# Kernel tuning notes

Hardware: AMD Instinct MI355X
Metric: run time of the kernel (lower is better)

Reference implementation:

```python
import jax, jax.numpy as jnp
import numpy as np

N_NODES, FEAT, EMB, BATCH, NUM_SAMPLE = 100000, 256, 256, 10000, 32


def setup_inputs() -> dict:
    key = jax.random.key(0)
    ks = jax.random.split(key, 8)
    sc = 1.0 / np.sqrt(FEAT).astype(np.float32)
    return {
        "nodes": jax.random.randint(ks[0], (BATCH,), 0, N_NODES),
        "neigh_idx": jax.random.randint(ks[1], (BATCH, NUM_SAMPLE), 0, N_NODES),
        "id2feat": jax.random.normal(ks[2], (N_NODES, FEAT), jnp.float32),
        "Wq": jax.random.normal(ks[3], (FEAT, EMB), jnp.float32) * sc,
        "bq": jnp.zeros((EMB,), jnp.float32),
        "Wk": jax.random.normal(ks[4], (FEAT, EMB), jnp.float32) * sc,
        "bk": jnp.zeros((EMB,), jnp.float32),
        "Wv": jax.random.normal(ks[5], (FEAT, EMB), jnp.float32) * sc,
        "bv": jnp.zeros((EMB,), jnp.float32),
    }


def reference(nodes, neigh_idx, id2feat, Wq, bq, Wk, bk, Wv, bv):
    # Gather: self feats [B, F] and sampled neighbor feats [B, S, F]
    self_feats = id2feat[nodes]
    neigh_feats = id2feat[neigh_idx]
    S = neigh_idx.shape[1]
    # Keys/values over [neighbors, self] -> [B, S+1, F]
    cat = jnp.concatenate([neigh_feats, self_feats[:, None, :]], axis=1)
    Q = self_feats @ Wq + bq               # [B, E]
    K = cat @ Wk + bk                       # [B, S+1, E]
    V = cat @ Wv + bv                       # [B, S+1, E]
    scores = jnp.einsum('be,bse->bs', Q, K)  # [B, S+1]
    # Faithful to original mask loop: with full neighbor lists, columns >= num_sample
    # (the appended self key) are masked out.
    mask = jnp.arange(S + 1) >= S
    scores = jnp.where(mask[None, :], -jnp.inf, scores)
    attn = jax.nn.softmax(scores, axis=-1)   # [B, S+1]
    return jnp.einsum('bs,bse->be', attn, V)  # [B, E]
```

## Files before the change

### kernel.cpp

```cpp
#include <hip/hip_runtime.h>
#include <math.h>

#define F 256
#define E 256
#define S 32
#define CH 4
#define LDK 40

typedef __attribute__((ext_vector_type(8))) short short8;
typedef __attribute__((ext_vector_type(4))) float f32x4;

__device__ __forceinline__ ushort f2bf(float x) {
    uint u = __float_as_uint(x);
    uint r = (u + 0x7fffu + ((u >> 16) & 1u)) >> 16;
    return (ushort)r;
}
__device__ __forceinline__ float bf2f(ushort h) {
    return __uint_as_float(((uint)h) << 16);
}

__global__ __launch_bounds__(256) void prep_all(const float* __restrict__ Wq,
                                                const float* __restrict__ bq,
                                                const float* __restrict__ Wk,
                                                const float* __restrict__ Wv,
                                                ushort* __restrict__ MT_hi,
                                                ushort* __restrict__ MT_lo,
                                                ushort* __restrict__ WvT_hi,
                                                ushort* __restrict__ WvT_lo,
                                                float* __restrict__ c) {
    const int t = threadIdx.x;
    if (blockIdx.x < 256) {
        const int j = blockIdx.x;
        __shared__ float wkj[F];
        wkj[t] = Wk[j * F + t];
        __syncthreads();
        float acc = 0.f;
#pragma unroll 8
        for (int e = 0; e < F; e += 4) {
            float4 wq = *reinterpret_cast<const float4*>(&Wq[t * E + e]);
            acc += wkj[e] * wq.x + wkj[e + 1] * wq.y + wkj[e + 2] * wq.z + wkj[e + 3] * wq.w;
        }
        const ushort hi = f2bf(acc);
        MT_hi[j * F + t] = hi;
        MT_lo[j * F + t] = f2bf(acc - bf2f(hi));
        if (t == 0) {
            float s = 0.f;
            for (int e = 0; e < F; ++e) s += wkj[e] * bq[e];
            c[j] = s;
        }
    } else {
        const int j = blockIdx.x - 256;
        const float v = Wv[t * E + j];
        const ushort hi = f2bf(v);
        WvT_hi[j * F + t] = hi;
        WvT_lo[j * F + t] = f2bf(v - bf2f(hi));
    }
}

__global__ __launch_bounds__(256) void mfma_gemm(const float* __restrict__ X,
                                                 const int* __restrict__ idx,
                                                 const ushort* __restrict__ BTh,
                                                 const ushort* __restrict__ BTl,
                                                 const float* __restrict__ bias,
                                                 float* __restrict__ out,
                                                 int rows) {
    __shared__ ushort Ah[64][LDK], Al[64][LDK];
    __shared__ ushort Bh[256][LDK], Bl[256][LDK];

    const int tid = threadIdx.x;
    const int lane = tid & 63, wave = tid >> 6;
    const int wm = wave >> 1, wn = wave & 1;
    const int fr = lane & 15, fk = lane >> 4;
    const int row0 = blockIdx.x * 64;

    const int arL = tid >> 2;
    const int akL = (tid & 3) * 8;
    const int ar = row0 + arL;
    const int arc = ar < rows ? ar : rows - 1;
    const long arow = idx ? (long)idx[arc] : (long)arc;
    const float* aptr = X + arow * (long)F + akL;

    const ushort* bhp = BTh + (size_t)tid * F;
    const ushort* blp = BTl + (size_t)tid * F;

    f32x4 acc[2][8];
#pragma unroll
    for (int m = 0; m < 2; ++m)
#pragma unroll
        for (int n = 0; n < 8; ++n) acc[m][n] = (f32x4){0.f, 0.f, 0.f, 0.f};

    for (int k0 = 0; k0 < F; k0 += 32) {
        const float4 v0 = *reinterpret_cast<const float4*>(&aptr[k0]);
        const float4 v1 = *reinterpret_cast<const float4*>(&aptr[k0 + 4]);
        const uint4 bh0 = *reinterpret_cast<const uint4*>(&bhp[k0]);
        const uint4 bh1 = *reinterpret_cast<const uint4*>(&bhp[k0 + 8]);
        const uint4 bh2 = *reinterpret_cast<const uint4*>(&bhp[k0 + 16]);
        const uint4 bh3 = *reinterpret_cast<const uint4*>(&bhp[k0 + 24]);
        const uint4 bl0 = *reinterpret_cast<const uint4*>(&blp[k0]);
        const uint4 bl1 = *reinterpret_cast<const uint4*>(&blp[k0 + 8]);
        const uint4 bl2 = *reinterpret_cast<const uint4*>(&blp[k0 + 16]);
        const uint4 bl3 = *reinterpret_cast<const uint4*>(&blp[k0 + 24]);

        const float xv[8] = {v0.x, v0.y, v0.z, v0.w, v1.x, v1.y, v1.z, v1.w};
        ushort h[8], l[8];
#pragma unroll
        for (int jj = 0; jj < 8; ++jj) {
            h[jj] = f2bf(xv[jj]);
            l[jj] = f2bf(xv[jj] - bf2f(h[jj]));
        }
        uint4 ph, pl;
        ph.x = (uint)h[0] | ((uint)h[1] << 16); ph.y = (uint)h[2] | ((uint)h[3] << 16);
        ph.z = (uint)h[4] | ((uint)h[5] << 16); ph.w = (uint)h[6] | ((uint)h[7] << 16);
        pl.x = (uint)l[0] | ((uint)l[1] << 16); pl.y = (uint)l[2] | ((uint)l[3] << 16);
        pl.z = (uint)l[4] | ((uint)l[5] << 16); pl.w = (uint)l[6] | ((uint)l[7] << 16);

        __syncthreads();
        *reinterpret_cast<uint4*>(&Ah[arL][akL]) = ph;
        *reinterpret_cast<uint4*>(&Al[arL][akL]) = pl;
        *reinterpret_cast<uint4*>(&Bh[tid][0])  = bh0;
        *reinterpret_cast<uint4*>(&Bh[tid][8])  = bh1;
        *reinterpret_cast<uint4*>(&Bh[tid][16]) = bh2;
        *reinterpret_cast<uint4*>(&Bh[tid][24]) = bh3;
        *reinterpret_cast<uint4*>(&Bl[tid][0])  = bl0;
        *reinterpret_cast<uint4*>(&Bl[tid][8])  = bl1;
        *reinterpret_cast<uint4*>(&Bl[tid][16]) = bl2;
        *reinterpret_cast<uint4*>(&Bl[tid][24]) = bl3;
        __syncthreads();

        const short8 a_h0 = *reinterpret_cast<const short8*>(&Ah[wm * 32 + fr][fk * 8]);
        const short8 a_l0 = *reinterpret_cast<const short8*>(&Al[wm * 32 + fr][fk * 8]);
        const short8 a_h1 = *reinterpret_cast<const short8*>(&Ah[wm * 32 + 16 + fr][fk * 8]);
        const short8 a_l1 = *reinterpret_cast<const short8*>(&Al[wm * 32 + 16 + fr][fk * 8]);
#pragma unroll
        for (int n = 0; n < 8; ++n) {
            const short8 b_h = *reinterpret_cast<const short8*>(&Bh[wn * 128 + n * 16 + fr][fk * 8]);
            const short8 b_l = *reinterpret_cast<const short8*>(&Bl[wn * 128 + n * 16 + fr][fk * 8]);
            acc[0][n] = __builtin_amdgcn_mfma_f32_16x16x32_bf16(a_h0, b_h, acc[0][n], 0, 0, 0);
            acc[0][n] = __builtin_amdgcn_mfma_f32_16x16x32_bf16(a_h0, b_l, acc[0][n], 0, 0, 0);
            acc[0][n] = __builtin_amdgcn_mfma_f32_16x16x32_bf16(a_l0, b_h, acc[0][n], 0, 0, 0);
            acc[1][n] = __builtin_amdgcn_mfma_f32_16x16x32_bf16(a_h1, b_h, acc[1][n], 0, 0, 0);
            acc[1][n] = __builtin_amdgcn_mfma_f32_16x16x32_bf16(a_h1, b_l, acc[1][n], 0, 0, 0);
            acc[1][n] = __builtin_amdgcn_mfma_f32_16x16x32_bf16(a_l1, b_h, acc[1][n], 0, 0, 0);
        }
    }

#pragma unroll
    for (int n = 0; n < 8; ++n) {
        const int col = wn * 128 + n * 16 + fr;
        const float bb = bias[col];
#pragma unroll
        for (int m = 0; m < 2; ++m) {
#pragma unroll
            for (int r = 0; r < 4; ++r) {
                const int orow = row0 + wm * 32 + m * 16 + fk * 4 + r;
                if (orow < rows)
                    out[(size_t)orow * E + col] = acc[m][n][r] + bb;
            }
        }
    }
}

__device__ __forceinline__ void ld_chunk(float4* d, int idxv, int s0,
                                         const float* __restrict__ t, int lane) {
#pragma unroll
    for (int j = 0; j < CH; ++j) {
        const int nid = __builtin_amdgcn_readlane(idxv, s0 + j);
        d[j] = *reinterpret_cast<const float4*>(&t[(size_t)nid * F + lane * 4]);
    }
}

__device__ __forceinline__ void proc_chunk(const float4* v, const float4 qv,
                                           float& m, float& l, float4& acc) {
#pragma unroll
    for (int j = 0; j < CH; ++j) {
        float p = v[j].x * qv.x + v[j].y * qv.y + v[j].z * qv.z + v[j].w * qv.w;
#pragma unroll
        for (int off = 32; off; off >>= 1) p += __shfl_xor(p, off);
        if (p <= m) {
            const float w = __expf(p - m);
            l += w;
            acc.x += w * v[j].x; acc.y += w * v[j].y;
            acc.z += w * v[j].z; acc.w += w * v[j].w;
        } else {
            const float c = __expf(m - p);
            l = l * c + 1.f;
            acc.x = acc.x * c + v[j].x; acc.y = acc.y * c + v[j].y;
            acc.z = acc.z * c + v[j].z; acc.w = acc.w * c + v[j].w;
            m = p;
        }
    }
}

__global__ __launch_bounds__(256) void attn_gather(const int* __restrict__ neigh_idx,
                                                   const float* __restrict__ id2feat,
                                                   float* __restrict__ qtm,
                                                   int B) {
    const int node = blockIdx.x * 4 + (threadIdx.x >> 6);
    const int lane = threadIdx.x & 63;
    if (node >= B) return;

    const int idxv = neigh_idx[node * S + (lane & (S - 1))];
    const float4 qv = *reinterpret_cast<const float4*>(&qtm[(size_t)node * F + lane * 4]);

    float m = -INFINITY, l = 0.f;
    float4 acc = make_float4(0.f, 0.f, 0.f, 0.f);

    float4 va[CH], vb[CH];
    ld_chunk(va, idxv, 0, id2feat, lane);
    ld_chunk(vb, idxv, 4, id2feat, lane);
    proc_chunk(va, qv, m, l, acc);
    ld_chunk(va, idxv, 8, id2feat, lane);
    proc_chunk(vb, qv, m, l, acc);
    ld_chunk(vb, idxv, 12, id2feat, lane);
    proc_chunk(va, qv, m, l, acc);
    ld_chunk(va, idxv, 16, id2feat, lane);
    proc_chunk(vb, qv, m, l, acc);
    ld_chunk(vb, idxv, 20, id2feat, lane);
    proc_chunk(va, qv, m, l, acc);
    ld_chunk(va, idxv, 24, id2feat, lane);
    proc_chunk(vb, qv, m, l, acc);
    ld_chunk(vb, idxv, 28, id2feat, lane);
    proc_chunk(va, qv, m, l, acc);
    proc_chunk(vb, qv, m, l, acc);

    const float inv = 1.0f / l;
    float4 o;
    o.x = acc.x * inv; o.y = acc.y * inv; o.z = acc.z * inv; o.w = acc.w * inv;
    *reinterpret_cast<float4*>(&qtm[(size_t)node * F + lane * 4]) = o;
}

extern "C" void kernel_launch(void* const* d_in, const int* in_sizes, int n_in,
                              void* d_out, int out_size, void* d_ws, size_t ws_size,
                              hipStream_t stream) {
    const int*   nodes   = (const int*)d_in[0];
    const int*   neigh   = (const int*)d_in[1];
    const float* id2feat = (const float*)d_in[2];
    const float* Wq      = (const float*)d_in[3];
    const float* bq      = (const float*)d_in[4];
    const float* Wk      = (const float*)d_in[5];
    const float* Wv      = (const float*)d_in[7];
    const float* bv      = (const float*)d_in[8];
    float* out = (float*)d_out;
    const int B = in_sizes[0];

    ushort* MT_hi  = (ushort*)d_ws;
    ushort* MT_lo  = MT_hi + 65536;
    ushort* WvT_hi = MT_lo + 65536;
    ushort* WvT_lo = WvT_hi + 65536;
    float*  cbuf   = (float*)(WvT_lo + 65536);
    float*  qtm    = cbuf + 256;

    prep_all<<<dim3(512), dim3(256), 0, stream>>>(Wq, bq, Wk, Wv,
                                                  MT_hi, MT_lo, WvT_hi, WvT_lo, cbuf);
    mfma_gemm<<<dim3((B + 63) / 64), dim3(256), 0, stream>>>(id2feat, nodes,
                                                             MT_hi, MT_lo, cbuf, qtm, B);
    attn_gather<<<dim3((B + 3) / 4), dim3(256), 0, stream>>>(neigh, id2feat, qtm, B);
    mfma_gemm<<<dim3((B + 63) / 64), dim3(256), 0, stream>>>(qtm, nullptr,
                                                             WvT_hi, WvT_lo, bv, out, B);
}
```

Before: 122.5 us.

## Compute Wk·Wqᵀ via MFMA GEMM, split prep kernel, widen GEMM blocks to 512 threads

```diff
diff --git a/kernel.cpp b/kernel.cpp
--- a/kernel.cpp
+++ b/kernel.cpp
@@ -12,151 +12,190 @@
 
 __device__ __forceinline__ ushort f2bf(float x) {
     uint u = __float_as_uint(x);
-    uint r = (u + 0x7fffu + ((u >> 16) & 1u)) >> 16;
-    return (ushort)r;
+    return (ushort)((u + 0x7fffu + ((u >> 16) & 1u)) >> 16);
 }
 __device__ __forceinline__ float bf2f(ushort h) {
     return __uint_as_float(((uint)h) << 16);
 }
-
-__global__ __launch_bounds__(256) void prep_all(const float* __restrict__ Wq,
-                                                const float* __restrict__ bq,
-                                                const float* __restrict__ Wk,
-                                                const float* __restrict__ Wv,
-                                                ushort* __restrict__ MT_hi,
-                                                ushort* __restrict__ MT_lo,
-                                                ushort* __restrict__ WvT_hi,
-                                                ushort* __restrict__ WvT_lo,
-                                                float* __restrict__ c) {
-    const int t = threadIdx.x;
-    if (blockIdx.x < 256) {
-        const int j = blockIdx.x;
-        __shared__ float wkj[F];
-        wkj[t] = Wk[j * F + t];
-        __syncthreads();
-        float acc = 0.f;
-#pragma unroll 8
-        for (int e = 0; e < F; e += 4) {
-            float4 wq = *reinterpret_cast<const float4*>(&Wq[t * E + e]);
-            acc += wkj[e] * wq.x + wkj[e + 1] * wq.y + wkj[e + 2] * wq.z + wkj[e + 3] * wq.w;
-        }
-        const ushort hi = f2bf(acc);
-        MT_hi[j * F + t] = hi;
-        MT_lo[j * F + t] = f2bf(acc - bf2f(hi));
-        if (t == 0) {
-            float s = 0.f;
-            for (int e = 0; e < F; ++e) s += wkj[e] * bq[e];
-            c[j] = s;
-        }
-    } else {
-        const int j = blockIdx.x - 256;
-        const float v = Wv[t * E + j];
-        const ushort hi = f2bf(v);
-        WvT_hi[j * F + t] = hi;
-        WvT_lo[j * F + t] = f2bf(v - bf2f(hi));
-    }
-}
-
-__global__ __launch_bounds__(256) void mfma_gemm(const float* __restrict__ X,
+__device__ __forceinline__ void split4(const float* x, uint2& ph, uint2& pl) {
+    ushort h[4], l[4];
+#pragma unroll
+    for (int i = 0; i < 4; ++i) { h[i] = f2bf(x[i]); l[i] = f2bf(x[i] - bf2f(h[i])); }
+    ph.x = (uint)h[0] | ((uint)h[1] << 16); ph.y = (uint)h[2] | ((uint)h[3] << 16);
+    pl.x = (uint)l[0] | ((uint)l[1] << 16); pl.y = (uint)l[2] | ((uint)l[3] << 16);
+}
+__device__ __forceinline__ uint4 pack8(const ushort* h) {
+    uint4 r;
+    r.x = (uint)h[0] | ((uint)h[1] << 16); r.y = (uint)h[2] | ((uint)h[3] << 16);
+    r.z = (uint)h[4] | ((uint)h[5] << 16); r.w = (uint)h[6] | ((uint)h[7] << 16);
+    return r;
+}
+
+template<bool INSPLIT, bool OUTSPLIT>
+__global__ __launch_bounds__(512) void mfma_gemm(const float* __restrict__ X,
                                                  const int* __restrict__ idx,
                                                  const ushort* __restrict__ BTh,
                                                  const ushort* __restrict__ BTl,
+                                                 const float* __restrict__ Bf,
                                                  const float* __restrict__ bias,
                                                  float* __restrict__ out,
+                                                 ushort* __restrict__ outh,
+                                                 ushort* __restrict__ outl,
                                                  int rows) {
     __shared__ ushort Ah[64][LDK], Al[64][LDK];
     __shared__ ushort Bh[256][LDK], Bl[256][LDK];
 
     const int tid = threadIdx.x;
     const int lane = tid & 63, wave = tid >> 6;
-    const int wm = wave >> 1, wn = wave & 1;
+    const int wm = wave >> 2, wn = wave & 3;
     const int fr = lane & 15, fk = lane >> 4;
     const int row0 = blockIdx.x * 64;
 
-    const int arL = tid >> 2;
-    const int akL = (tid & 3) * 8;
+    const int arL = tid >> 3;
+    const int akL = (tid & 7) * 4;
     const int ar = row0 + arL;
     const int arc = ar < rows ? ar : rows - 1;
     const long arow = idx ? (long)idx[arc] : (long)arc;
     const float* aptr = X + arow * (long)F + akL;
 
-    const ushort* bhp = BTh + (size_t)tid * F;
-    const ushort* blp = BTl + (size_t)tid * F;
-
-    f32x4 acc[2][8];
+    const int bcol = tid & 255;
+    const int bkh = (tid >> 8) * 16;
+
+    f32x4 acc[2][4];
 #pragma unroll
     for (int m = 0; m < 2; ++m)
 #pragma unroll
-        for (int n = 0; n < 8; ++n) acc[m][n] = (f32x4){0.f, 0.f, 0.f, 0.f};
+        for (int n = 0; n < 4; ++n) acc[m][n] = (f32x4){0.f, 0.f, 0.f, 0.f};
 
     for (int k0 = 0; k0 < F; k0 += 32) {
-        const float4 v0 = *reinterpret_cast<const float4*>(&aptr[k0]);
-        const float4 v1 = *reinterpret_cast<const float4*>(&aptr[k0 + 4]);
-        const uint4 bh0 = *reinterpret_cast<const uint4*>(&bhp[k0]);
-        const uint4 bh1 = *reinterpret_cast<const uint4*>(&bhp[k0 + 8]);
-        const uint4 bh2 = *reinterpret_cast<const uint4*>(&bhp[k0 + 16]);
-        const uint4 bh3 = *reinterpret_cast<const uint4*>(&bhp[k0 + 24]);
-        const uint4 bl0 = *reinterpret_cast<const uint4*>(&blp[k0]);
-        const uint4 bl1 = *reinterpret_cast<const uint4*>(&blp[k0 + 8]);
-        const uint4 bl2 = *reinterpret_cast<const uint4*>(&blp[k0 + 16]);
-        const uint4 bl3 = *reinterpret_cast<const uint4*>(&blp[k0 + 24]);
-
-        const float xv[8] = {v0.x, v0.y, v0.z, v0.w, v1.x, v1.y, v1.z, v1.w};
-        ushort h[8], l[8];
-#pragma unroll
-        for (int jj = 0; jj < 8; ++jj) {
-            h[jj] = f2bf(xv[jj]);
-            l[jj] = f2bf(xv[jj] - bf2f(h[jj]));
-        }
-        uint4 ph, pl;
-        ph.x = (uint)h[0] | ((uint)h[1] << 16); ph.y = (uint)h[2] | ((uint)h[3] << 16);
-        ph.z = (uint)h[4] | ((uint)h[5] << 16); ph.w = (uint)h[6] | ((uint)h[7] << 16);
-        pl.x = (uint)l[0] | ((uint)l[1] << 16); pl.y = (uint)l[2] | ((uint)l[3] << 16);
-        pl.z = (uint)l[4] | ((uint)l[5] << 16); pl.w = (uint)l[6] | ((uint)l[7] << 16);
+        const float4 av = *reinterpret_cast<const float4*>(&aptr[k0]);
+        uint2 ah, al;
+        split4(&av.x, ah, al);
+
+        uint4 wh0, wh1, wl0, wl1;
+        if constexpr (INSPLIT) {
+            const float* bp = Bf + (size_t)bcol * F + k0 + bkh;
+            float4 b0 = *reinterpret_cast<const float4*>(bp);
+            float4 b1 = *reinterpret_cast<const float4*>(bp + 4);
+            float4 b2 = *reinterpret_cast<const float4*>(bp + 8);
+            float4 b3 = *reinterpret_cast<const float4*>(bp + 12);
+            uint2 h0, l0, h1, l1, h2, l2, h3, l3;
+            split4(&b0.x, h0, l0); split4(&b1.x, h1, l1);
+            split4(&b2.x, h2, l2); split4(&b3.x, h3, l3);
+            wh0 = make_uint4(h0.x, h0.y, h1.x, h1.y);
+            wh1 = make_uint4(h2.x, h2.y, h3.x, h3.y);
+            wl0 = make_uint4(l0.x, l0.y, l1.x, l1.y);
+            wl1 = make_uint4(l2.x, l2.y, l3.x, l3.y);
+        } else {
+            const ushort* bph = BTh + (size_t)bcol * F + k0 + bkh;
+            const ushort* bpl = BTl + (size_t)bcol * F + k0 + bkh;
+            wh0 = *reinterpret_cast<const uint4*>(bph);
+            wh1 = *reinterpret_cast<const uint4*>(bph + 8);
+            wl0 = *reinterpret_cast<const uint4*>(bpl);
+            wl1 = *reinterpret_cast<const uint4*>(bpl + 8);
+        }
 
         __syncthreads();
-        *reinterpret_cast<uint4*>(&Ah[arL][akL]) = ph;
-        *reinterpret_cast<uint4*>(&Al[arL][akL]) = pl;
-        *reinterpret_cast<uint4*>(&Bh[tid][0])  = bh0;
-        *reinterpret_cast<uint4*>(&Bh[tid][8])  = bh1;
-        *reinterpret_cast<uint4*>(&Bh[tid][16]) = bh2;
-        *reinterpret_cast<uint4*>(&Bh[tid][24]) = bh3;
-        *reinterpret_cast<uint4*>(&Bl[tid][0])  = bl0;
-        *reinterpret_cast<uint4*>(&Bl[tid][8])  = bl1;
-        *reinterpret_cast<uint4*>(&Bl[tid][16]) = bl2;
-        *reinterpret_cast<uint4*>(&Bl[tid][24]) = bl3;
+        *reinterpret_cast<uint2*>(&Ah[arL][akL]) = ah;
+        *reinterpret_cast<uint2*>(&Al[arL][akL]) = al;
+        *reinterpret_cast<uint4*>(&Bh[bcol][bkh]) = wh0;
+        *reinterpret_cast<uint4*>(&Bh[bcol][bkh + 8]) = wh1;
+        *reinterpret_cast<uint4*>(&Bl[bcol][bkh]) = wl0;
+        *reinterpret_cast<uint4*>(&Bl[bcol][bkh + 8]) = wl1;
         __syncthreads();
 
-        const short8 a_h0 = *reinterpret_cast<const short8*>(&Ah[wm * 32 + fr][fk * 8]);
-        const short8 a_l0 = *reinterpret_cast<const short8*>(&Al[wm * 32 + fr][fk * 8]);
-        const short8 a_h1 = *reinterpret_cast<const short8*>(&Ah[wm * 32 + 16 + fr][fk * 8]);
-        const short8 a_l1 = *reinterpret_cast<const short8*>(&Al[wm * 32 + 16 + fr][fk * 8]);
-#pragma unroll
-        for (int n = 0; n < 8; ++n) {
-            const short8 b_h = *reinterpret_cast<const short8*>(&Bh[wn * 128 + n * 16 + fr][fk * 8]);
-            const short8 b_l = *reinterpret_cast<const short8*>(&Bl[wn * 128 + n * 16 + fr][fk * 8]);
-            acc[0][n] = __builtin_amdgcn_mfma_f32_16x16x32_bf16(a_h0, b_h, acc[0][n], 0, 0, 0);
-            acc[0][n] = __builtin_amdgcn_mfma_f32_16x16x32_bf16(a_h0, b_l, acc[0][n], 0, 0, 0);
-            acc[0][n] = __builtin_amdgcn_mfma_f32_16x16x32_bf16(a_l0, b_h, acc[0][n], 0, 0, 0);
-            acc[1][n] = __builtin_amdgcn_mfma_f32_16x16x32_bf16(a_h1, b_h, acc[1][n], 0, 0, 0);
-            acc[1][n] = __builtin_amdgcn_mfma_f32_16x16x32_bf16(a_h1, b_l, acc[1][n], 0, 0, 0);
-            acc[1][n] = __builtin_amdgcn_mfma_f32_16x16x32_bf16(a_l1, b_h, acc[1][n], 0, 0, 0);
-        }
-    }
-
-#pragma unroll
-    for (int n = 0; n < 8; ++n) {
-        const int col = wn * 128 + n * 16 + fr;
-        const float bb = bias[col];
+        short8 a_h[2], a_l[2];
+#pragma unroll
+        for (int m = 0; m < 2; ++m) {
+            a_h[m] = *reinterpret_cast<const short8*>(&Ah[wm * 32 + m * 16 + fr][fk * 8]);
+            a_l[m] = *reinterpret_cast<const short8*>(&Al[wm * 32 + m * 16 + fr][fk * 8]);
+        }
+#pragma unroll
+        for (int n = 0; n < 4; ++n) {
+            const short8 b_h = *reinterpret_cast<const short8*>(&Bh[wn * 64 + n * 16 + fr][fk * 8]);
+            const short8 b_l = *reinterpret_cast<const short8*>(&Bl[wn * 64 + n * 16 + fr][fk * 8]);
+#pragma unroll
+            for (int m = 0; m < 2; ++m) {
+                acc[m][n] = __builtin_amdgcn_mfma_f32_16x16x32_bf16(a_h[m], b_h, acc[m][n], 0, 0, 0);
+                acc[m][n] = __builtin_amdgcn_mfma_f32_16x16x32_bf16(a_h[m], b_l, acc[m][n], 0, 0, 0);
+                acc[m][n] = __builtin_amdgcn_mfma_f32_16x16x32_bf16(a_l[m], b_h, acc[m][n], 0, 0, 0);
+            }
+        }
+    }
+
+#pragma unroll
+    for (int n = 0; n < 4; ++n) {
+        const int col = wn * 64 + n * 16 + fr;
+        float bb = 0.f;
+        if constexpr (!OUTSPLIT) bb = bias[col];
 #pragma unroll
         for (int m = 0; m < 2; ++m) {
 #pragma unroll
             for (int r = 0; r < 4; ++r) {
                 const int orow = row0 + wm * 32 + m * 16 + fk * 4 + r;
-                if (orow < rows)
-                    out[(size_t)orow * E + col] = acc[m][n][r] + bb;
+                if (orow < rows) {
+                    if constexpr (OUTSPLIT) {
+                        const float v = acc[m][n][r];
+                        const ushort h = f2bf(v);
+                        outh[(size_t)orow * F + col] = h;
+                        outl[(size_t)orow * F + col] = f2bf(v - bf2f(h));
+                    } else {
+                        out[(size_t)orow * E + col] = acc[m][n][r] + bb;
+                    }
+                }
             }
         }
+    }
+}
+
+__global__ __launch_bounds__(256) void prep_misc(const float* __restrict__ Wk,
+                                                 const float* __restrict__ bq,
+                                                 const float* __restrict__ Wv,
+                                                 float* __restrict__ c,
+                                                 ushort* __restrict__ WvTh,
+                                                 ushort* __restrict__ WvTl) {
+    if (blockIdx.x < 4) {
+        __shared__ float bqs[F];
+        bqs[threadIdx.x] = bq[threadIdx.x];
+        __syncthreads();
+        const int lane = threadIdx.x & 63, w = threadIdx.x >> 6;
+        const float4 b4 = *reinterpret_cast<const float4*>(&bqs[lane * 4]);
+#pragma unroll
+        for (int i = 0; i < 16; ++i) {
+            const int j = blockIdx.x * 64 + w * 16 + i;
+            const float4 k4 = *reinterpret_cast<const float4*>(&Wk[(size_t)j * F + lane * 4]);
+            float p = k4.x * b4.x + k4.y * b4.y + k4.z * b4.z + k4.w * b4.w;
+#pragma unroll
+            for (int off = 32; off; off >>= 1) p += __shfl_xor(p, off);
+            if (lane == 0) c[j] = p;
+        }
+    } else {
+        __shared__ float t[64][65];
+        const int tb = blockIdx.x - 4;
+        const int jt = (tb & 3) * 64, kt = (tb >> 2) * 64;
+        const int lk = threadIdx.x >> 2;
+        const int lj = (threadIdx.x & 3) * 16;
+#pragma unroll
+        for (int u = 0; u < 16; u += 4) {
+            const float4 v = *reinterpret_cast<const float4*>(&Wv[(size_t)(kt + lk) * E + jt + lj + u]);
+            t[lk][lj + u] = v.x; t[lk][lj + u + 1] = v.y;
+            t[lk][lj + u + 2] = v.z; t[lk][lj + u + 3] = v.w;
+        }
+        __syncthreads();
+        const int oj = threadIdx.x >> 2;
+        const int ok = (threadIdx.x & 3) * 16;
+        ushort h[16], l[16];
+#pragma unroll
+        for (int u = 0; u < 16; ++u) {
+            const float v = t[ok + u][oj];
+            h[u] = f2bf(v); l[u] = f2bf(v - bf2f(h[u]));
+        }
+        ushort* ph = &WvTh[(size_t)(jt + oj) * F + kt + ok];
+        ushort* pl = &WvTl[(size_t)(jt + oj) * F + kt + ok];
+        *reinterpret_cast<uint4*>(ph) = pack8(h);
+        *reinterpret_cast<uint4*>(ph + 8) = pack8(h + 8);
+        *reinterpret_cast<uint4*>(pl) = pack8(l);
+        *reinterpret_cast<uint4*>(pl + 8) = pack8(l + 8);
     }
 }
 
@@ -182,10 +221,10 @@
             acc.x += w * v[j].x; acc.y += w * v[j].y;
             acc.z += w * v[j].z; acc.w += w * v[j].w;
         } else {
-            const float c = __expf(m - p);
-            l = l * c + 1.f;
-            acc.x = acc.x * c + v[j].x; acc.y = acc.y * c + v[j].y;
-            acc.z = acc.z * c + v[j].z; acc.w = acc.w * c + v[j].w;
+            const float cc = __expf(m - p);
+            l = l * cc + 1.f;
+            acc.x = acc.x * cc + v[j].x; acc.y = acc.y * cc + v[j].y;
+            acc.z = acc.z * cc + v[j].z; acc.w = acc.w * cc + v[j].w;
             m = p;
         }
     }
@@ -250,11 +289,12 @@
     float*  cbuf   = (float*)(WvT_lo + 65536);
     float*  qtm    = cbuf + 256;
 
-    prep_all<<<dim3(512), dim3(256), 0, stream>>>(Wq, bq, Wk, Wv,
-                                                  MT_hi, MT_lo, WvT_hi, WvT_lo, cbuf);
-    mfma_gemm<<<dim3((B + 63) / 64), dim3(256), 0, stream>>>(id2feat, nodes,
-                                                             MT_hi, MT_lo, cbuf, qtm, B);
+    mfma_gemm<true, true><<<dim3(4), dim3(512), 0, stream>>>(
+        Wk, nullptr, nullptr, nullptr, Wq, nullptr, nullptr, MT_hi, MT_lo, 256);
+    prep_misc<<<dim3(20), dim3(256), 0, stream>>>(Wk, bq, Wv, cbuf, WvT_hi, WvT_lo);
+    mfma_gemm<false, false><<<dim3((B + 63) / 64), dim3(512), 0, stream>>>(
+        id2feat, nodes, MT_hi, MT_lo, nullptr, cbuf, qtm, nullptr, nullptr, B);
     attn_gather<<<dim3((B + 3) / 4), dim3(256), 0, stream>>>(neigh, id2feat, qtm, B);
-    mfma_gemm<<<dim3((B + 63) / 64), dim3(256), 0, stream>>>(qtm, nullptr,
-                                                             WvT_hi, WvT_lo, bv, out, B);
-}
+    mfma_gemm<false, false><<<dim3((B + 63) / 64), dim3(512), 0, stream>>>(
+        qtm, nullptr, WvT_hi, WvT_lo, nullptr, bv, out, nullptr, nullptr, B);
+}
```

Measured after the change: 123.0 us. No clear change (+0.3%).
